# Kernel tuning notes

Measured on AMD Instinct MI355X. Metric: run time of the kernel, lower is better.

## Reference

```python
import jax, jax.numpy as jnp
import numpy as np

MAP_X = 72; MAP_Y = 72      # global map grid
R = 300                      # number of rooms
MAXS = 8                     # rooms padded to 8x8 (zero-padded occupancy)
E = 32                       # room_embedding_width
N = 128                      # batch
CONV_CH = [64, 128, 256]; KS = [5, 3, 3]
FC = [512, 256]; OUT_W = 512


def setup_inputs() -> dict:
    key = jax.random.key(0)
    ks = jax.random.split(key, 20)
    rng = np.random.default_rng(0)
    widths = rng.integers(1, MAXS + 1, R)
    heights = rng.integers(1, MAXS + 1, R)
    # room_maps[i] is room.map transposed -> [width, height], zero-padded to [MAXS, MAXS]
    rm = np.zeros((R, MAXS, MAXS), np.int32)
    for i in range(R):
        rm[i, :widths[i], :heights[i]] = rng.integers(0, 2, (int(widths[i]), int(heights[i])))
    inp = {}
    # room top-left positions; rooms fit since max size is MAXS
    inp["X"] = jax.random.randint(ks[0], (N, R, 2), 0, MAP_X - MAXS + 1, dtype=jnp.int32)
    inp["room_maps"] = jnp.asarray(rm)
    inp["room_emb"] = jax.random.normal(ks[1], (R, E), jnp.float32)
    cin = [1 + E] + CONV_CH
    for i in range(3):
        k = KS[i]; fan = cin[i] * k * k
        inp[f"conv_w{i}"] = jax.random.normal(ks[2 + 2 * i], (cin[i + 1], cin[i], k, k), jnp.float32) / np.sqrt(fan).astype(np.float32)
        inp[f"conv_b{i}"] = jnp.zeros((cin[i + 1],), jnp.float32)
    fcd = [CONV_CH[-1]] + FC + [OUT_W]
    for i in range(3):
        inp[f"fc_w{i}"] = jax.random.normal(ks[10 + 2 * i], (fcd[i + 1], fcd[i]), jnp.float32) / np.sqrt(fcd[i]).astype(np.float32)
        inp[f"fc_b{i}"] = jnp.zeros((fcd[i + 1],), jnp.float32)
    return inp


def _encode_map(X, room_maps, room_emb):
    # Fused scatter: occupancy channel + embedding channels scattered in one pass.
    rm = room_maps.astype(room_emb.dtype)                    # [R, W, H]
    vals = jnp.concatenate(
        [rm[..., None], rm[..., None] * room_emb[:, None, None, :]], axis=-1
    )                                                        # [R, W, H, 1+E]
    ax = jnp.arange(MAXS)

    def one(pos):  # pos: [R, 2] positions for one batch element
        ix = jnp.broadcast_to(pos[:, 0, None, None] + ax[None, :, None], (R, MAXS, MAXS))
        iy = jnp.broadcast_to(pos[:, 1, None, None] + ax[None, None, :], (R, MAXS, MAXS))
        grid = jnp.zeros((MAP_X, MAP_Y, 1 + E), vals.dtype)
        # padded cells are zero so dropped/duplicate adds are exact
        return grid.at[ix, iy].add(vals, mode="drop")

    out = jax.vmap(one)(X)                                   # [N, MAP_X, MAP_Y, 1+E]
    # torch: transpose(1,3) -> [N, 1+E, MAP_Y, MAP_X]
    return jnp.transpose(out, (0, 3, 2, 1))


def _conv_relu(x, w, b, k):
    p = k // 2
    y = jax.lax.conv_general_dilated(
        x, w, (1, 1), [(p, p), (p, p)], dimension_numbers=("NCHW", "OIHW", "NCHW"))
    return jax.nn.relu(y + b[None, :, None, None])


def _maxpool3s2(x):
    return jax.lax.reduce_window(x, -jnp.inf, jax.lax.max, (1, 1, 3, 3), (1, 1, 2, 2), "VALID")


def reference(X, room_maps, room_emb, conv_w0, conv_b0, conv_w1, conv_b1, conv_w2, conv_b2, fc_w0, fc_b0, fc_w1, fc_b1, fc_w2, fc_b2):
    x = _encode_map(X, room_maps, room_emb)
    for w, b, k in ((conv_w0, conv_b0, KS[0]), (conv_w1, conv_b1, KS[1]), (conv_w2, conv_b2, KS[2])):
        x = _maxpool3s2(_conv_relu(x, w, b, k))
    x = jnp.mean(x, axis=(2, 3))                             # GlobalAvgPool2d
    x = jax.nn.relu(x @ fc_w0.T + fc_b0)
    x = jax.nn.relu(x @ fc_w1.T + fc_b1)
    return x @ fc_w2.T + fc_b2
```

## Files before the change

### kernel.cpp

```cpp
#include <hip/hip_runtime.h>
#include <hip/hip_bf16.h>
#include <cstdint>
#include <cstddef>

#define NB      128
#define RR      300
#define EMB     32

typedef __bf16 bf16x8 __attribute__((ext_vector_type(8)));
typedef float  f32x4  __attribute__((ext_vector_type(4)));
typedef unsigned short ushort8 __attribute__((ext_vector_type(8)));

__device__ __forceinline__ unsigned short f2bf(float f) {
    union { __hip_bfloat16 h; unsigned short u; } c;
    c.h = __float2bfloat16(f);
    return c.u;
}
__device__ __forceinline__ float bf2f(unsigned short u) {
    union { __hip_bfloat16 h; unsigned short u; } c;
    c.u = u;
    return __bfloat162float(c.h);
}

__device__ __forceinline__ void wpack_body(
    const float* __restrict__ w, unsigned short* __restrict__ wPT,
    int COUT, int CIN, int KK, int gpc, int idx, int total)
{
    if (idx >= total) return;
    int kk = idx & 31;
    int t  = idx >> 5;
    int oc = t % COUT;
    int kb = t / COUT;
    int g  = kb * 4 + (kk >> 3);
    int j  = kk & 7;
    int shift = g / gpc;
    int ci    = (g % gpc) * 8 + j;
    float v = (shift < KK && ci < CIN)
        ? w[(size_t)oc * CIN * KK + (size_t)ci * KK + shift] : 0.0f;
    wPT[idx] = f2bf(v);
}

__device__ __forceinline__ void fcT_body(
    const float* __restrict__ w, float* __restrict__ wT, int O, int I, int idx)
{
    if (idx >= O * I) return;
    int i = idx % I, o = idx / I;
    wT[(size_t)i * O + o] = w[idx];
}

__global__ __launch_bounds__(256) void prep_k(
    const int* __restrict__ rm, unsigned long long* __restrict__ masks,
    const float* __restrict__ cw0, unsigned short* __restrict__ WP0,
    const float* __restrict__ cw1, unsigned short* __restrict__ WP1,
    const float* __restrict__ cw2, unsigned short* __restrict__ WP2,
    int* __restrict__ kt0, int* __restrict__ kt1, int* __restrict__ kt2,
    const float* __restrict__ fw0, float* __restrict__ W0T,
    const float* __restrict__ fw1, float* __restrict__ W1T,
    const float* __restrict__ fw2, float* __restrict__ W2T)
{
    const int b = blockIdx.x;
    const int t = threadIdx.x;
    if (b < 2) {
        int r = b * 256 + t;
        if (r < RR) {
            unsigned long long m = 0ull;
            #pragma unroll
            for (int k = 0; k < 64; ++k)
                if (rm[r * 64 + k]) m |= (1ull << k);
            masks[r] = m;
        }
    } else if (b < 258) {
        wpack_body(cw0, WP0, 64, 33, 25, 5, (b - 2) * 256 + t, 32 * 64 * 32);
    } else if (b < 546) {
        wpack_body(cw1, WP1, 128, 64, 9, 8, (b - 258) * 256 + t, 18 * 128 * 32);
    } else if (b < 1698) {
        wpack_body(cw2, WP2, 256, 128, 9, 16, (b - 546) * 256 + t, 36 * 256 * 32);
    } else if (b < 1699) {
        #pragma unroll
        for (int which = 0; which < 3; ++which) {
            int ngr, gpc, K, Wp, CL;
            int* dst;
            if (which == 0)      { ngr = 128; gpc = 5;  K = 5; Wp = 20; CL = 40;  dst = kt0; }
            else if (which == 1) { ngr = 72;  gpc = 8;  K = 3; Wp = 37; CL = 72;  dst = kt1; }
            else                 { ngr = 144; gpc = 16; K = 3; Wp = 19; CL = 136; dst = kt2; }
            if (t < ngr) {
                int shift = t / gpc;
                int off = 0;
                if (shift < K * K) {
                    int ky = shift / K, kx = shift % K;
                    off = (ky * Wp + kx) * CL + (t % gpc) * 8;
                }
                dst[t] = off;
            }
        }
    } else if (b < 2211) {
        fcT_body(fw0, W0T, 512, 256, (b - 1699) * 256 + t);
    } else if (b < 2723) {
        fcT_body(fw1, W1T, 256, 512, (b - 2211) * 256 + t);
    } else {
        fcT_body(fw2, W2T, 512, 256, (b - 2723) * 256 + t);
    }
}

__device__ __forceinline__ void border_body(
    unsigned short* __restrict__ base, int Hp, int Wp, int CPG, int pad,
    int sampleStride, int nborder, int idx, int total)
{
    if (idx >= total) return;
    int c8 = idx % CPG;
    int t  = idx / CPG;
    int bi = t % nborder;
    int nl = t / nborder;

    int topN = pad * Wp;
    int y, x;
    if (bi < topN) {
        y = bi / Wp; x = bi - y * Wp;
    } else if (bi < 2 * topN) {
        int b2 = bi - topN;
        y = Hp - pad + b2 / Wp; x = b2 % Wp;
    } else {
        int mid = bi - 2 * topN;
        int rowlen = 2 * pad;
        y = pad + mid / rowlen;
        int r = mid % rowlen;
        x = r < pad ? r : Wp - pad + (r - pad);
    }
    uint4 z = make_uint4(0, 0, 0, 0);
    *reinterpret_cast<uint4*>(
        &base[((size_t)nl * sampleStride) +
              ((size_t)y * Wp + x) * (CPG * 8) + c8 * 8]) = z;
}

__global__ __launch_bounds__(576) void encode_k(
    const int* __restrict__ X, const unsigned long long* __restrict__ masks,
    const float* __restrict__ emb, unsigned short* __restrict__ G,
    int n0, int sampleStride)
{
    __shared__ float s_emb[RR * 36];
    __shared__ unsigned s_pos[RR];
    __shared__ unsigned long long s_mask[RR];
    __shared__ unsigned short s_list[320];
    __shared__ int s_woff[9];
    __shared__ int s_cnt;

    const int nl = blockIdx.x, band = blockIdx.y;
    const int by = band * 8;
    const int n  = n0 + nl;
    const int tid = threadIdx.x;

    for (int i = tid; i < RR * 36; i += 576) {
        int r = i / 36, c = i - r * 36;
        float v = 0.0f;
        if (c == 0) v = 1.0f;
        else if (c < 33) v = emb[r * EMB + c - 1];
        s_emb[i] = v;
    }

    const int2* Xp = reinterpret_cast<const int2*>(X);
    bool hot = false;
    if (tid < RR) {
        int2 pos = Xp[n * RR + tid];
        s_pos[tid]  = (unsigned)pos.x | ((unsigned)pos.y << 16);
        s_mask[tid] = masks[tid];
        hot = (pos.y <= by + 7) && (pos.y + 7 >= by);
    }
    unsigned long long bal = __ballot(hot);
    if ((tid & 63) == 0) s_woff[tid >> 6] = (int)__popcll(bal);
    __syncthreads();
    if (tid == 0) {
        int acc = 0;
        #pragma unroll
        for (int w = 0; w < 9; ++w) { int c = s_woff[w]; s_woff[w] = acc; acc += c; }
        s_cnt = acc;
    }
    __syncthreads();
    if (hot) {
        int w = tid >> 6, b = tid & 63;
        unsigned long long before = (b == 0) ? 0ull : (bal & ((1ull << b) - 1ull));
        s_list[s_woff[w] + (int)__popcll(before)] = (unsigned short)tid;
    }
    __syncthreads();

    const int x  = tid % 72;
    const int Y  = by + tid / 72;

    f32x4 acc[9];
    #pragma unroll
    for (int k = 0; k < 9; ++k) acc[k] = (f32x4){0.f, 0.f, 0.f, 0.f};

    const int cnt = s_cnt;
    for (int idx = 0; idx < cnt; ++idx) {
        int r = s_list[idx];
        unsigned pxy = s_pos[r];
        int dxr = x - (int)(pxy & 0xffffu);
        int dyr = Y - (int)(pxy >> 16);
        if (((unsigned)dxr < 8u) && ((unsigned)dyr < 8u) &&
            ((s_mask[r] >> (dxr * 8 + dyr)) & 1ull)) {
            const f32x4* er = reinterpret_cast<const f32x4*>(&s_emb[r * 36]);
            #pragma unroll
            for (int k = 0; k < 9; ++k) acc[k] += er[k];
        }
    }

    unsigned short* Gn = G + (size_t)nl * sampleStride;
    {
        unsigned short o[40];
        #pragma unroll
        for (int k = 0; k < 9; ++k)
            #pragma unroll
            for (int j = 0; j < 4; ++j)
                o[k * 4 + j] = f2bf(acc[k][j]);
        #pragma unroll
        for (int c = 36; c < 40; ++c) o[c] = 0;
        uint4* dst = reinterpret_cast<uint4*>(
            &Gn[((size_t)(Y + 2) * 76 + (x + 2)) * 40]);
        const uint4* src = reinterpret_cast<const uint4*>(o);
        #pragma unroll
        for (int q = 0; q < 5; ++q) dst[q] = src[q];
    }

    uint4 zz4; zz4.x = zz4.y = zz4.z = zz4.w = 0;
    if (tid < 160) {
        int q = tid % 5, cell = tid / 5;
        int ci = cell & 3, rr = cell >> 2;
        int xx = ci < 2 ? ci : 72 + ci;
        uint4* dst = reinterpret_cast<uint4*>(
            &Gn[((size_t)(by + rr + 2) * 76 + xx) * 40]);
        dst[q] = zz4;
    }
    if (band == 0 || band == 8) {
        int rbase = band == 0 ? 0 : 74;
        for (int i = tid; i < 2 * 76 * 5; i += 576) {
            int q = i % 5, cell = i / 5;
            int xx = cell % 76, rr = cell / 76;
            uint4* dst = reinterpret_cast<uint4*>(
                &Gn[((size_t)(rbase + rr) * 76 + xx) * 40]);
            dst[q] = zz4;
        }
    }
}

template<int KSTEPS>
__global__ __launch_bounds__(256, 3) void conv0_tile_k(
    const unsigned short* __restrict__ inP,
    const unsigned short* __restrict__ wPT,
    const int* __restrict__ ktab,
    const float* __restrict__ bias,
    unsigned short* __restrict__ out,
    int inSS, int outSS)
{
    constexpr int CL = 40;
    constexpr int LP = 72;
    __shared__ __align__(16) unsigned short slab[28 * 20 * CL];
    __shared__ __align__(16) unsigned short wbuf[2][2048];
    __shared__ int s_kt[KSTEPS * 4];
    unsigned short* s_c = slab;

    const int tid = threadIdx.x;
    const int tl  = blockIdx.x;
    const int nl  = blockIdx.y;
    const int tyi = tl / 5, txi = tl % 5;
    const int y0 = tyi * 24;
    const int x0 = txi < 4 ? txi * 16 : 56;

    const int lane = tid & 63, wv = tid >> 6, frow = lane & 15, fq = lane >> 4;

    if (tid < KSTEPS * 4) s_kt[tid] = ktab[tid];

    {
        const unsigned short* src = wPT + wv * 512 + lane * 8;
        __builtin_amdgcn_global_load_lds(
            (const __attribute__((address_space(1))) void*)src,
            (__attribute__((address_space(3))) void*)&wbuf[0][wv * 512],
            16, 0, 0);
    }

    const unsigned short* in_n = inP + (size_t)nl * inSS;
    {
        const uint4* src = reinterpret_cast<const uint4*>(in_n);
        uint4* dst = reinterpret_cast<uint4*>(slab);
        #pragma unroll
        for (int it = 0; it < 11; ++it) {
            int q = tid + it * 256;
            if (q < 2800) {
                int r = q / 100, c = q - r * 100;
                dst[q] = src[((y0 + r) * 76 + x0) * 5 + c];
            }
        }
    }

    int ldsb[6];
    #pragma unroll
    for (int mf = 0; mf < 6; ++mf)
        ldsb[mf] = ((mf * 4 + wv) * 20 + frow) * CL;

    f32x4 acc[6][4];
    #pragma unroll
    for (int a = 0; a < 6; ++a)
        #pragma unroll
        for (int b = 0; b < 4; ++b) acc[a][b] = (f32x4){0.f, 0.f, 0.f, 0.f};

    __syncthreads();

    #pragma unroll 2
    for (int kb = 0; kb < KSTEPS; ++kb) {
        const int cur = kb & 1;
        if (kb + 1 < KSTEPS) {
            const unsigned short* src =
                wPT + (size_t)(kb + 1) * 2048 + wv * 512 + lane * 8;
            __builtin_amdgcn_global_load_lds(
                (const __attribute__((address_space(1))) void*)src,
                (__attribute__((address_space(3))) void*)&wbuf[cur ^ 1][wv * 512],
                16, 0, 0);
        }
        int go = s_kt[kb * 4 + fq];
        bf16x8 af[6];
        #pragma unroll
        for (int mf = 0; mf < 6; ++mf)
            af[mf] = *reinterpret_cast<const bf16x8*>(&slab[ldsb[mf] + go]);
        const unsigned short* wl = &wbuf[cur][frow * 32 + fq * 8];
        #pragma unroll
        for (int ng = 0; ng < 4; ++ng) {
            bf16x8 bf = *reinterpret_cast<const bf16x8*>(&wl[ng * 512]);
            #pragma unroll
            for (int mf = 0; mf < 6; ++mf)
                acc[mf][ng] = __builtin_amdgcn_mfma_f32_16x16x32_bf16(
                    af[mf], bf, acc[mf][ng], 0, 0, 0);
        }
        __syncthreads();
    }

    unsigned short* out_n = out + (size_t)nl * outSS;
    const int erow = tid >> 2, eseg = tid & 3;
    #pragma unroll
    for (int mf = 0; mf < 6; ++mf) {
        __syncthreads();
        #pragma unroll
        for (int ng = 0; ng < 4; ++ng) {
            float bv = bias[ng * 16 + frow];
            #pragma unroll
            for (int j = 0; j < 4; ++j)
                s_c[(wv * 16 + fq * 4 + j) * LP + ng * 16 + frow] =
                    f2bf(fmaxf(acc[mf][ng][j] + bv, 0.0f));
        }
        __syncthreads();
        {
            int ty = mf * 4 + (erow >> 4);
            int tx = erow & 15;
            int pos = (y0 + ty) * 72 + (x0 + tx);
            ushort8 v0 = *reinterpret_cast<const ushort8*>(
                &s_c[erow * LP + eseg * 16]);
            ushort8 v1 = *reinterpret_cast<const ushort8*>(
                &s_c[erow * LP + eseg * 16 + 8]);
            unsigned short* op = out_n + (size_t)pos * 64 + eseg * 16;
            *reinterpret_cast<ushort8*>(op) = v0;
            *reinterpret_cast<ushort8*>(op + 8) = v1;
        }
    }
}

template<int MFRAG, int NG, int KH, int CPG, int CL, int SLAB, int KSTEPS>
__global__ __launch_bounds__(256, 2) void conv_mfma_k(
    const unsigned short* __restrict__ inP,
    const unsigned short* __restrict__ wPT,
    const int* __restrict__ ktab,
    const float* __restrict__ bias,
    unsigned short* __restrict__ out,
    int W, int Wp, int Mtot, int inSS, int outSS, int COUT)
{
    constexpr int Mblk = MFRAG * 64;
    constexpr int NOC  = NG * 16;
    constexpr int SEGS = NOC / 16;
    constexpr int LP   = NOC + 8;
    constexpr int CP   = CPG * 8;
    constexpr int CSZ  = Mblk * LP * 2;
    constexpr int SMEM = (SLAB * 2 > CSZ) ? SLAB * 2 : CSZ;
    __shared__ __align__(16) char smem[SMEM];
    __shared__ int s_kt[KSTEPS * 4];
    unsigned short* slab = reinterpret_cast<unsigned short*>(smem);
    unsigned short* s_c  = reinterpret_cast<unsigned short*>(smem);

    const int tid  = threadIdx.x;
    const int mb   = blockIdx.x;
    const int ocb  = blockIdx.y;
    const int nl   = blockIdx.z;
    const int lane = tid & 63;
    const int wv   = tid >> 6;
    const int frow = lane & 15;
    const int fq   = lane >> 4;

    if (tid < KSTEPS * 4) s_kt[tid] = ktab[tid];

    const int p0    = mb * Mblk;
    const int y0    = p0 / W;
    const int plast = (p0 + Mblk < Mtot ? p0 + Mblk : Mtot) - 1;
    const int rows  = plast / W - y0 + KH;

    const unsigned short* in_n =
        inP + (size_t)nl * inSS + (size_t)y0 * Wp * CP;
    const int nchunks = rows * Wp * CPG;
    for (int q = tid; q < nchunks; q += 256) {
        int pix = q / CPG, c8 = q - pix * CPG;
        uint4 v = reinterpret_cast<const uint4*>(in_n)[q];
        *reinterpret_cast<uint4*>(&slab[pix * CL + c8 * 8]) = v;
    }

    int ldsb[MFRAG];
    #pragma unroll
    for (int mf = 0; mf < MFRAG; ++mf) {
        int p  = p0 + mf * 64 + wv * 16 + frow;
        int pc = p < Mtot ? p : (Mtot - 1);
        int y  = pc / W;
        int x  = pc - y * W;
        ldsb[mf] = ((y - y0) * Wp + x) * CL;
    }
    const unsigned short* wbase =
        wPT + ((size_t)(ocb * NOC + frow)) * 32 + fq * 8;

    f32x4 acc[MFRAG][NG];
    #pragma unroll
    for (int mf = 0; mf < MFRAG; ++mf)
        #pragma unroll
        for (int ng = 0; ng < NG; ++ng)
            acc[mf][ng] = (f32x4){0.f, 0.f, 0.f, 0.f};

    __syncthreads();

    for (int kb = 0; kb < KSTEPS; ++kb) {
        int go = s_kt[kb * 4 + fq];
        bf16x8 af[MFRAG];
        #pragma unroll
        for (int mf = 0; mf < MFRAG; ++mf)
            af[mf] = *reinterpret_cast<const bf16x8*>(&slab[ldsb[mf] + go]);
        const unsigned short* wk = wbase + (size_t)kb * COUT * 32;
        #pragma unroll
        for (int ng = 0; ng < NG; ++ng) {
            bf16x8 bf = *reinterpret_cast<const bf16x8*>(wk + ng * 16 * 32);
            #pragma unroll
            for (int mf = 0; mf < MFRAG; ++mf)
                acc[mf][ng] = __builtin_amdgcn_mfma_f32_16x16x32_bf16(
                    af[mf], bf, acc[mf][ng], 0, 0, 0);
        }
    }

    __syncthreads();
    #pragma unroll
    for (int mf = 0; mf < MFRAG; ++mf) {
        #pragma unroll
        for (int ng = 0; ng < NG; ++ng) {
            float bv = bias[ocb * NOC + ng * 16 + frow];
            #pragma unroll
            for (int j = 0; j < 4; ++j)
                s_c[(mf * 64 + wv * 16 + fq * 4 + j) * LP + ng * 16 + frow] =
                    f2bf(fmaxf(acc[mf][ng][j] + bv, 0.0f));
        }
    }
    __syncthreads();
    unsigned short* out_n = out + (size_t)nl * outSS;
    for (int t = tid; t < Mblk * SEGS; t += 256) {
        int row = t / SEGS, seg = t - row * SEGS;
        int p = p0 + row;
        if (p < Mtot) {
            ushort8 v0 = *reinterpret_cast<const ushort8*>(
                &s_c[row * LP + seg * 16]);
            ushort8 v1 = *reinterpret_cast<const ushort8*>(
                &s_c[row * LP + seg * 16 + 8]);
            unsigned short* op =
                out_n + (size_t)p * COUT + ocb * NOC + seg * 16;
            *reinterpret_cast<ushort8*>(op) = v0;
            *reinterpret_cast<ushort8*>(op + 8) = v1;
        }
    }
}

__global__ __launch_bounds__(256) void pool_border_k(
    const unsigned short* __restrict__ in, unsigned short* __restrict__ out,
    int CG, int C, int W, int inSS,
    int HO, int WO, int Wpo, int outSS, int total,
    int npool, int bHp, int bWp, int bCPG, int bpad, int bnborder, int btotal)
{
    const int b = blockIdx.x;
    const int tidx = threadIdx.x;
    if (b >= npool) {
        border_body(out, bHp, bWp, bCPG, bpad, outSS, bnborder,
                    (b - npool) * 256 + tidx, btotal);
        return;
    }
    int idx = b * 256 + tidx;
    if (idx >= total) return;
    int cg = idx % CG;
    int t  = idx / CG;
    int x  = t % WO;
    t /= WO;
    int y  = t % HO;
    int nl = t / HO;

    const unsigned short* pin = in + (size_t)nl * inSS + cg * 8;
    ushort8 mx = {0,0,0,0,0,0,0,0};
    #pragma unroll
    for (int dy = 0; dy < 3; ++dy)
        #pragma unroll
        for (int dx = 0; dx < 3; ++dx) {
            ushort8 v = *reinterpret_cast<const ushort8*>(
                pin + ((size_t)(2 * y + dy) * W + (2 * x + dx)) * C);
            #pragma unroll
            for (int j = 0; j < 8; ++j) mx[j] = v[j] > mx[j] ? v[j] : mx[j];
        }
    *reinterpret_cast<ushort8*>(
        out + (size_t)nl * outSS +
        ((size_t)(y + 1) * Wpo + (x + 1)) * C + cg * 8) = mx;
}

__global__ __launch_bounds__(256) void pool2gap_k(
    const unsigned short* __restrict__ in, float* __restrict__ out,
    int inSS, int n0)
{
    __shared__ float red[4][4][8];
    const int nl = blockIdx.x;
    const int cg = blockIdx.y;
    const int tid = threadIdx.x;
    const int w  = tid >> 2;
    const int cq = tid & 3;
    const int y = w >> 3, x = w & 7;

    const unsigned short* p = in + (size_t)nl * inSS + cg * 32 + cq * 8;
    ushort8 mx = {0,0,0,0,0,0,0,0};
    #pragma unroll
    for (int dy = 0; dy < 3; ++dy)
        #pragma unroll
        for (int dx = 0; dx < 3; ++dx) {
            ushort8 v = *reinterpret_cast<const ushort8*>(
                p + ((size_t)(2 * y + dy) * 17 + (2 * x + dx)) * 256);
            #pragma unroll
            for (int j = 0; j < 8; ++j) mx[j] = v[j] > mx[j] ? v[j] : mx[j];
        }
    float s[8];
    #pragma unroll
    for (int j = 0; j < 8; ++j) s[j] = bf2f(mx[j]);
    #pragma unroll
    for (int m = 4; m < 64; m <<= 1)
        #pragma unroll
        for (int j = 0; j < 8; ++j)
            s[j] += __shfl_xor(s[j], m);
    if ((tid & 63) < 4) {
        #pragma unroll
        for (int j = 0; j < 8; ++j) red[tid >> 6][tid & 3][j] = s[j];
    }
    __syncthreads();
    if (tid < 32) {
        int cq2 = tid >> 3, j = tid & 7;
        float t = red[0][cq2][j] + red[1][cq2][j] + red[2][cq2][j] + red[3][cq2][j];
        out[(size_t)(n0 + nl) * 256 + cg * 32 + cq2 * 8 + j] = t * (1.0f / 64.0f);
    }
}

__global__ __launch_bounds__(256) void fc_fused_k(
    const float* __restrict__ in,
    const float* __restrict__ w0T, const float* __restrict__ b0,
    const float* __restrict__ w1T, const float* __restrict__ b1,
    const float* __restrict__ w2T, const float* __restrict__ b2,
    float* __restrict__ out)
{
    __shared__ float s_in[256], s_h0[512], s_h1[256];
    const int n = blockIdx.x, t = threadIdx.x;
    s_in[t] = in[(size_t)n * 256 + t];
    __syncthreads();
    float a0 = 0.f, a1 = 0.f;
    for (int i = 0; i < 256; ++i) {
        float v = s_in[i];
        a0 += v * w0T[i * 512 + t];
        a1 += v * w0T[i * 512 + t + 256];
    }
    s_h0[t]       = fmaxf(a0 + b0[t], 0.0f);
    s_h0[t + 256] = fmaxf(a1 + b0[t + 256], 0.0f);
    __syncthreads();
    float h = 0.f;
    for (int i = 0; i < 512; ++i) h += s_h0[i] * w1T[i * 256 + t];
    s_h1[t] = fmaxf(h + b1[t], 0.0f);
    __syncthreads();
    a0 = 0.f; a1 = 0.f;
    for (int i = 0; i < 256; ++i) {
        float v = s_h1[i];
        a0 += v * w2T[i * 512 + t];
        a1 += v * w2T[i * 512 + t + 256];
    }
    out[(size_t)n * 512 + t]       = a0 + b2[t];
    out[(size_t)n * 512 + t + 256] = a1 + b2[t + 256];
}

extern "C" void kernel_launch(void* const* d_in, const int* in_sizes, int n_in,
                              void* d_out, int out_size, void* d_ws, size_t ws_size,
                              hipStream_t stream)
{
    const int*   X   = (const int*)d_in[0];
    const int*   rm  = (const int*)d_in[1];
    const float* emb = (const float*)d_in[2];
    const float* cw0 = (const float*)d_in[3];
    const float* cb0 = (const float*)d_in[4];
    const float* cw1 = (const float*)d_in[5];
    const float* cb1 = (const float*)d_in[6];
    const float* cw2 = (const float*)d_in[7];
    const float* cb2 = (const float*)d_in[8];
    const float* fw0 = (const float*)d_in[9];
    const float* fb0 = (const float*)d_in[10];
    const float* fw1 = (const float*)d_in[11];
    const float* fb1 = (const float*)d_in[12];
    const float* fw2 = (const float*)d_in[13];
    const float* fb2 = (const float*)d_in[14];
    float* out = (float*)d_out;

    char* p = (char*)d_ws;
    auto alloc = [&](size_t bytes) -> char* {
        char* r = p; p += (bytes + 255) & ~(size_t)255; return r;
    };
    unsigned short* WP0 = (unsigned short*)alloc((size_t)32 * 64 * 32 * 2);
    unsigned short* WP1 = (unsigned short*)alloc((size_t)18 * 128 * 32 * 2);
    unsigned short* WP2 = (unsigned short*)alloc((size_t)36 * 256 * 32 * 2);
    int* KT0 = (int*)alloc(128 * 4);
    int* KT1 = (int*)alloc(72 * 4);
    int* KT2 = (int*)alloc(144 * 4);
    unsigned long long* MASKS = (unsigned long long*)alloc(RR * 8);
    float* W0T  = (float*)alloc((size_t)256 * 512 * 4);
    float* W1T  = (float*)alloc((size_t)512 * 256 * 4);
    float* W2T  = (float*)alloc((size_t)256 * 512 * 4);
    float* GAPB = (float*)alloc((size_t)NB * 256 * 4);
    size_t fixed_bytes = (size_t)(p - (char*)d_ws);

    const size_t A_FL = 231040, B_FL = 331776, C_FL = 133824;
    const size_t per_sample = (A_FL + B_FL + C_FL) * 2 + 768;
    int Bc = 128;
    while (Bc > 1 && fixed_bytes + (size_t)Bc * per_sample > ws_size) Bc >>= 1;

    unsigned short* bufA = (unsigned short*)alloc((size_t)Bc * A_FL * 2);
    unsigned short* bufC = (unsigned short*)alloc((size_t)Bc * C_FL * 2);
    unsigned short* bufB = (unsigned short*)alloc((size_t)Bc * B_FL * 2);

    prep_k<<<3235, 256, 0, stream>>>(
        rm, MASKS, cw0, WP0, cw1, WP1, cw2, WP2,
        KT0, KT1, KT2, fw0, W0T, fw1, W1T, fw2, W2T);

    for (int n0 = 0; n0 < NB; n0 += Bc) {
        encode_k<<<dim3(Bc, 9), 576, 0, stream>>>(X, MASKS, emb, bufA, n0, (int)A_FL);

        conv0_tile_k<32><<<dim3(15, Bc), 256, 0, stream>>>(
            bufA, WP0, KT0, cb0, bufB, (int)A_FL, (int)B_FL);

        {
            int total = Bc * 35 * 35 * 8;
            int npool = (total + 255) / 256;
            int btotal = Bc * 144 * 8;
            int nbord = (btotal + 255) / 256;
            pool_border_k<<<npool + nbord, 256, 0, stream>>>(
                bufB, bufC, 8, 64, 72, (int)B_FL,
                35, 35, 37, (int)C_FL, total,
                npool, 37, 37, 8, 1, 144, btotal);
        }

        conv_mfma_k<4, 8, 3, 8, 72, 29304, 18><<<dim3(5, 1, Bc), 256, 0, stream>>>(
            bufC, WP1, KT1, cb1, bufA, 35, 37,
            1225, (int)C_FL, (int)A_FL, 128);

        {
            int total = Bc * 17 * 17 * 16;
            int npool = (total + 255) / 256;
            int btotal = Bc * 72 * 16;
            int nbord = (btotal + 255) / 256;
            pool_border_k<<<npool + nbord, 256, 0, stream>>>(
                bufA, bufC + 87616, 16, 128, 35, (int)A_FL,
                17, 17, 19, (int)C_FL, total,
                npool, 19, 19, 16, 1, 72, btotal);
        }

        conv_mfma_k<5, 8, 3, 16, 136, 49096, 36><<<dim3(1, 2, Bc), 256, 0, stream>>>(
            bufC + 87616, WP2, KT2, cb2, bufB, 17, 19,
            289, (int)C_FL, (int)B_FL, 256);

        pool2gap_k<<<dim3(Bc, 8), 256, 0, stream>>>(bufB, GAPB, (int)B_FL, n0);
    }

    fc_fused_k<<<NB, 256, 0, stream>>>(GAPB, W0T, fb0, W1T, fb1, W2T, fb2, out);
}
```

Before: 420.1 us.

## Stream conv0 weights from global into a 4-deep register prefetch ring

The conv0 tile kernel no longer stages weight slices through a double-buffered LDS buffer. Each lane now loads its weight fragments straight from global memory into four rotating register sets, prefetching four k-steps ahead. This removes the per-k-step __syncthreads and the LDS weight traffic. In exchange it uses more registers, so launch bounds drop from 3 to 2 blocks per SM, and the weights are re-read through the cache by every block. The unconditional steps assume KSTEPS is a multiple of 4.

```diff
diff --git a/kernel.cpp b/kernel.cpp
--- a/kernel.cpp
+++ b/kernel.cpp
@@ -242,7 +242,7 @@
 }
 
 template<int KSTEPS>
-__global__ __launch_bounds__(256, 3) void conv0_tile_k(
+__global__ __launch_bounds__(256, 2) void conv0_tile_k(
     const unsigned short* __restrict__ inP,
     const unsigned short* __restrict__ wPT,
     const int* __restrict__ ktab,
@@ -253,7 +253,6 @@
     constexpr int CL = 40;
     constexpr int LP = 72;
     __shared__ __align__(16) unsigned short slab[28 * 20 * CL];
-    __shared__ __align__(16) unsigned short wbuf[2][2048];
     __shared__ int s_kt[KSTEPS * 4];
     unsigned short* s_c = slab;
 
@@ -268,14 +267,6 @@
 
     if (tid < KSTEPS * 4) s_kt[tid] = ktab[tid];
 
-    {
-        const unsigned short* src = wPT + wv * 512 + lane * 8;
-        __builtin_amdgcn_global_load_lds(
-            (const __attribute__((address_space(1))) void*)src,
-            (__attribute__((address_space(3))) void*)&wbuf[0][wv * 512],
-            16, 0, 0);
-    }
-
     const unsigned short* in_n = inP + (size_t)nl * inSS;
     {
         const uint4* src = reinterpret_cast<const uint4*>(in_n);
@@ -295,40 +286,44 @@
     for (int mf = 0; mf < 6; ++mf)
         ldsb[mf] = ((mf * 4 + wv) * 20 + frow) * CL;
 
+    const unsigned short* wbase = wPT + (size_t)frow * 32 + fq * 8;
+
     f32x4 acc[6][4];
     #pragma unroll
     for (int a = 0; a < 6; ++a)
         #pragma unroll
         for (int b = 0; b < 4; ++b) acc[a][b] = (f32x4){0.f, 0.f, 0.f, 0.f};
 
-    __syncthreads();
-
-    #pragma unroll 2
-    for (int kb = 0; kb < KSTEPS; ++kb) {
-        const int cur = kb & 1;
-        if (kb + 1 < KSTEPS) {
-            const unsigned short* src =
-                wPT + (size_t)(kb + 1) * 2048 + wv * 512 + lane * 8;
-            __builtin_amdgcn_global_load_lds(
-                (const __attribute__((address_space(1))) void*)src,
-                (__attribute__((address_space(3))) void*)&wbuf[cur ^ 1][wv * 512],
-                16, 0, 0);
-        }
+    bf16x8 wa[4], wb[4], wc[4], wd[4];
+    auto LOADW = [&](bf16x8 (&w)[4], int kb) {
+        const unsigned short* p = wbase + (size_t)kb * 2048;
+        #pragma unroll
+        for (int ng = 0; ng < 4; ++ng)
+            w[ng] = *reinterpret_cast<const bf16x8*>(p + ng * 512);
+    };
+    auto STEP = [&](int kb, bf16x8 (&w)[4]) {
         int go = s_kt[kb * 4 + fq];
         bf16x8 af[6];
         #pragma unroll
         for (int mf = 0; mf < 6; ++mf)
             af[mf] = *reinterpret_cast<const bf16x8*>(&slab[ldsb[mf] + go]);
-        const unsigned short* wl = &wbuf[cur][frow * 32 + fq * 8];
-        #pragma unroll
-        for (int ng = 0; ng < 4; ++ng) {
-            bf16x8 bf = *reinterpret_cast<const bf16x8*>(&wl[ng * 512]);
+        #pragma unroll
+        for (int ng = 0; ng < 4; ++ng)
             #pragma unroll
             for (int mf = 0; mf < 6; ++mf)
                 acc[mf][ng] = __builtin_amdgcn_mfma_f32_16x16x32_bf16(
-                    af[mf], bf, acc[mf][ng], 0, 0, 0);
-        }
-        __syncthreads();
+                    af[mf], w[ng], acc[mf][ng], 0, 0, 0);
+    };
+
+    LOADW(wa, 0); LOADW(wb, 1); LOADW(wc, 2); LOADW(wd, 3);
+
+    __syncthreads();
+
+    for (int kb = 0; kb < KSTEPS; kb += 4) {
+        STEP(kb + 0, wa); if (kb + 4 < KSTEPS) LOADW(wa, kb + 4);
+        STEP(kb + 1, wb); if (kb + 5 < KSTEPS) LOADW(wb, kb + 5);
+        STEP(kb + 2, wc); if (kb + 6 < KSTEPS) LOADW(wc, kb + 6);
+        STEP(kb + 3, wd); if (kb + 7 < KSTEPS) LOADW(wd, kb + 7);
     }
 
     unsigned short* out_n = out + (size_t)nl * outSS;
```

Result: no change. 418.5 us (-0.4%).
